# Performance work log

Hardware: AMD Instinct MI355X
Metric: run time of the kernel (lower is better)

Reference implementation:

```python
import jax, jax.numpy as jnp
import numpy as np

_BN = 1.0 / np.sqrt(1.0 + 1e-5)  # eval-mode BatchNorm1d with default (fresh-init) stats/affine

def bn(z):
    return z * _BN

def lrelu(z, a):
    return jnp.where(z >= 0, z, a * z)

NEG = -9e15

def setup_inputs() -> dict:
    key = jax.random.key(0)
    ks = jax.random.split(key, 20)
    H = Wd = 256; B = 200; N = 2048; NHID = 128; OUT = 64; HEADS = 4
    x = jax.random.normal(ks[0], (H, Wd, B), dtype=jnp.float32)
    Q = jax.random.uniform(ks[1], (H * Wd, N), dtype=jnp.float32)
    adj = (jax.random.uniform(ks[2], (N, N)) < 0.02).astype(jnp.float32)
    adj = jnp.maximum(adj, jnp.eye(N, dtype=jnp.float32))  # self loops so no empty rows
    def u(k, shape, fan):
        s = 1.0 / np.sqrt(fan)
        return jax.random.uniform(k, shape, jnp.float32, -s, s)
    inp = dict(x=x, adj=adj, Q=Q)
    inp['g1a_W'] = u(ks[3], (B, NHID), NHID);  inp['g1a_b'] = u(ks[4], (NHID,), NHID)
    inp['g1b_W'] = u(ks[5], (NHID, B), B);     inp['g1b_b'] = u(ks[6], (B,), B)
    inp['g2a_W'] = u(ks[7], (B, NHID), NHID);  inp['g2a_b'] = u(ks[8], (NHID,), NHID)
    inp['g2b_W'] = u(ks[9], (NHID, OUT), OUT); inp['g2b_b'] = u(ks[10], (OUT,), OUT)
    inp['gat_W'] = jax.random.normal(ks[11], (HEADS, B, NHID)) * 0.1
    inp['gat_a'] = jax.random.normal(ks[12], (HEADS, 2 * NHID)) * 0.1
    inp['out_W'] = jax.random.normal(ks[13], (HEADS * NHID, OUT)) * 0.1
    inp['out_a'] = jax.random.normal(ks[14], (2 * OUT,)) * 0.1
    inp['Wf'] = u(ks[15], (2, OUT), OUT)
    inp['bf'] = u(ks[16], (2, OUT), OUT)
    inp['conv_w'] = jax.random.normal(ks[17], (3,)) * 0.5
    inp['conv_b'] = jax.random.normal(ks[18], (1,)) * 0.1
    return inp

def reference(x, adj, Q, g1a_W, g1a_b, g1b_W, g1b_b, g2a_W, g2a_b, g2b_W, g2b_b,
              gat_W, gat_a, out_W, out_a, Wf, bf, conv_w, conv_b):
    HW = x.shape[0] * x.shape[1]
    xf = x.reshape(HW, -1)                                   # [HW, C]
    normQ = Q / jnp.sum(Q, axis=0, keepdims=True)            # column-normalized assignment
    sp = normQ.T @ xf                                        # [N, C] superpixel features
    xn = bn(sp)

    # ---- Res_GCN branch ----
    def gcn_block(z, Wa, ba, Wb, bb):
        z = bn(z)
        z = lrelu(adj @ (z @ Wa) + ba, 0.01)
        z = bn(z)
        return adj @ (z @ Wb) + bb

    xg = bn(xn)
    y = lrelu(bn(gcn_block(xg, g1a_W, g1a_b, g1b_W, g1b_b)), 0.01)
    xg = xg + y
    GCN_x = lrelu(bn(gcn_block(xg, g2a_W, g2a_b, g2b_W, g2b_b)), 0.01)  # [N, OUT]

    # ---- GAT branch (fused pairwise scores: e_ij = lrelu(a1.Wh_i + a2.Wh_j)) ----
    mask = adj > 0
    nhid = gat_W.shape[2]

    def gat_head(Wk, ak):
        Wh = xn @ Wk                                         # [N, nhid]
        f1 = Wh @ ak[:nhid]                                  # [N]
        f2 = Wh @ ak[nhid:]                                  # [N]
        e = lrelu(f1[:, None] + f2[None, :], 0.2)            # [N, N]
        att = jax.nn.softmax(jnp.where(mask, e, NEG), axis=1)
        return jax.nn.elu(att @ Wh)                          # concat=True -> ELU

    heads = jax.vmap(gat_head)(gat_W, gat_a)                 # [H, N, nhid]
    hcat = jnp.moveaxis(heads, 0, 1).reshape(heads.shape[1], -1)  # [N, H*nhid]

    fo = out_W.shape[1]
    Wh = hcat @ out_W                                        # [N, OUT]
    e = lrelu((Wh @ out_a[:fo])[:, None] + (Wh @ out_a[fo:])[None, :], 0.2)
    att = jax.nn.softmax(jnp.where(mask, e, NEG), axis=1)
    GAT_x = lrelu(bn(jax.nn.elu(att @ Wh)), 0.01)            # [N, OUT]

    # ---- adaptive fusion ----
    mn = jnp.minimum(GCN_x, GAT_x)
    mx = jnp.maximum(GCN_x, GAT_x)
    avg = (GCN_x * Wf[0] + bf[0]) + (GAT_x * Wf[1] + bf[1])
    stk = jnp.stack([mn, mx, avg], axis=0)                   # [3, N, OUT]
    inp3 = stk + GAT_x + GCN_x                               # broadcast add
    y = jnp.einsum('c,cnf->nf', conv_w, inp3) + conv_b       # 1x1 conv 3->1 channels
    y = lrelu(bn(y), 0.2)                                    # AF2GNN1 leakyrelu(alpha)
    return Q @ y                                             # [HW, OUT]
```

## Files before the change

kernel.cpp:

```cpp
#include <hip/hip_runtime.h>
#include <math.h>

#define BNF 0.9999950000374997f

constexpr int N    = 2048;
constexpr int C    = 200;
constexpr int HW   = 65536;
constexpr int MAXDEG = 96;

typedef unsigned short u16;
typedef __attribute__((ext_vector_type(8))) short short8;
typedef __attribute__((ext_vector_type(4))) float f32x4;

union Frag  { short8 v; ushort4 h[2]; };
union FragA { short8 v; uint2 u2[2]; };

__device__ inline u16 f2bf(float x) {
    unsigned int u = __float_as_uint(x);
    unsigned int r = (u + 0x7fffu + ((u >> 16) & 1u)) >> 16;
    return (u16)r;
}

__device__ __forceinline__ void gload16(const void* g, void* l) {
    __builtin_amdgcn_global_load_lds(
        (const __attribute__((address_space(1))) unsigned int*)g,
        (__attribute__((address_space(3))) unsigned int*)l, 16, 0, 0);
}

__global__ __launch_bounds__(256) void k_convX(const float* __restrict__ xf,
                                               u16* __restrict__ xfT) {
    __shared__ __align__(16) u16 T2[200][140];
    const int i0 = blockIdx.x * 128;
    const int t = threadIdx.x;
    for (int p = 0; p < 25; ++p) {
        int idx = p * 256 + t;
        int il = idx / 50, cq = idx % 50;
        float4 v = *(const float4*)&xf[(size_t)(i0 + il) * 200 + cq * 4];
        T2[cq * 4 + 0][il] = f2bf(v.x);
        T2[cq * 4 + 1][il] = f2bf(v.y);
        T2[cq * 4 + 2][il] = f2bf(v.z);
        T2[cq * 4 + 3][il] = f2bf(v.w);
    }
    __syncthreads();
    for (int p = 0; p < 13; ++p) {
        int c = p * 16 + (t >> 4);
        if (c < 200) {
            int io = (t & 15) * 8;
            u16* dst = &xfT[(size_t)c * 65536 + i0 + io];
            *(ushort4*)&dst[0] = *(const ushort4*)&T2[c][io];
            *(ushort4*)&dst[4] = *(const ushort4*)&T2[c][io + 4];
        }
    }
    ushort4 z4 = {0, 0, 0, 0};
    for (int idx = t; idx < 8 * 16; idx += 256) {
        int r = 200 + (idx >> 4), io = (idx & 15) * 8;
        u16* dst = &xfT[(size_t)r * 65536 + i0 + io];
        *(ushort4*)&dst[0] = z4;
        *(ushort4*)&dst[4] = z4;
    }
}

__global__ __launch_bounds__(256, 3) void k_bigS(const float* __restrict__ Q,
                                                 const u16* __restrict__ xfT,
                                                 u16* __restrict__ Qbf,
                                                 float* __restrict__ S_part,
                                                 float* __restrict__ csPart) {
    __shared__ __align__(16) u16 Bt[2][208 * 32];
    __shared__ __align__(16) u16 At[64 * 34];
    const int bid = blockIdx.x;
    const int xcd = bid & 7, jb = bid >> 3;
    const int nt_b = jb & 31;
    const int ks_b = ((jb >> 5) << 3) + xcd;
    const int n0 = nt_b * 64;
    const size_t i0 = (size_t)ks_b * 2048;
    const int t = threadIdx.x, w = t >> 6, l = t & 63;
    const int ct0 = (w == 0) ? 0 : (4 + (w - 1) * 3);
    const int nct = (w == 0) ? 4 : 3;
    const int lrowB = l >> 2;
    const int scolB = (((l & 3) ^ ((l >> 3) & 3)) << 3);
    const int nq = t & 15;
    const int kp = t >> 4;

    f32x4 acc[4][4];
#pragma unroll
    for (int a = 0; a < 4; ++a)
#pragma unroll
        for (int b = 0; b < 4; ++b) acc[a][b] = (f32x4){0.f, 0.f, 0.f, 0.f};
    float csum[4] = {0.f, 0.f, 0.f, 0.f};

    float4 aq0, ar0, aq1, ar1;

#define ISSUE_B(PAR, STEP)                                                      \
    {                                                                           \
        const size_t kc = i0 + (size_t)(STEP) * 32 + scolB;                     \
        for (int s = w; s < 13; s += 4)                                         \
            gload16(&xfT[(size_t)(s * 16 + lrowB) * 65536 + kc],                \
                    &Bt[PAR][s * 512]);                                         \
    }

#define LOAD_A(AQ, AR, STEP)                                                    \
    {                                                                           \
        const float* qp = &Q[(i0 + (size_t)(STEP) * 32 + kp * 2) * 2048         \
                             + n0 + nq * 4];                                    \
        AQ = *(const float4*)qp;                                                \
        AR = *(const float4*)(qp + 2048);                                       \
    }

#define WRITE_A(AQ, AR, STEP)                                                   \
    {                                                                           \
        const float* ca = (const float*)&AQ;                                    \
        const float* cb = (const float*)&AR;                                    \
        ushort4 s0, s1;                                                         \
        u16* q0 = (u16*)&s0; u16* q1 = (u16*)&s1;                               \
        _Pragma("unroll")                                                       \
        for (int jj = 0; jj < 4; ++jj) {                                        \
            const int n_ = nq * 4 + jj;                                         \
            ushort2 p2;                                                         \
            p2.x = f2bf(ca[jj]); p2.y = f2bf(cb[jj]);                           \
            *(ushort2*)&At[n_ * 34 + ((n_ & 1) << 1) + kp * 2] = p2;            \
            csum[jj] += ca[jj] + cb[jj];                                        \
            q0[jj] = p2.x; q1[jj] = p2.y;                                       \
        }                                                                       \
        const size_t r0 = i0 + (size_t)(STEP) * 32 + kp * 2;                    \
        *(ushort4*)&Qbf[r0 * 2048 + n0 + nq * 4] = s0;                          \
        *(ushort4*)&Qbf[(r0 + 1) * 2048 + n0 + nq * 4] = s1;                    \
    }

#define MFMA_PHASE(PAR)                                                         \
    {                                                                           \
        const u16* Bb = Bt[PAR];                                                \
        const int g = l >> 4;                                                   \
        FragA af[4];                                                            \
        _Pragma("unroll")                                                       \
        for (int nt = 0; nt < 4; ++nt) {                                        \
            const int r = nt * 16 + (l & 15);                                   \
            const int ab = r * 34 + ((r & 1) << 1) + g * 8;                     \
            af[nt].u2[0] = *(const uint2*)&At[ab];                              \
            af[nt].u2[1] = *(const uint2*)&At[ab + 4];                          \
        }                                                                       \
        _Pragma("unroll")                                                       \
        for (int c = 0; c < 4; ++c) {                                           \
            if (c < nct) {                                                      \
                const int rb = (ct0 + c) * 16 + (l & 15);                       \
                Frag bf;                                                        \
                bf.v = *(const short8*)&Bb[rb * 32 + ((g ^ ((rb >> 1) & 3)) << 3)]; \
                _Pragma("unroll")                                               \
                for (int nt = 0; nt < 4; ++nt)                                  \
                    acc[nt][c] = __builtin_amdgcn_mfma_f32_16x16x32_bf16(       \
                        af[nt].v, bf.v, acc[nt][c], 0, 0, 0);                   \
            }                                                                   \
        }                                                                       \
    }

#define STEPBODY(STEP, PAR, NPAR, CQ, CR, NQr, NRr, COND)                       \
    {                                                                           \
        if (COND) ISSUE_B(NPAR, (STEP) + 1);                                    \
        WRITE_A(CQ, CR, STEP);                                                  \
        if (COND) LOAD_A(NQr, NRr, (STEP) + 1);                                 \
        asm volatile("s_waitcnt lgkmcnt(0)" ::: "memory");                      \
        __builtin_amdgcn_s_barrier();                                           \
        if (COND) {                                                             \
            if (w == 0) asm volatile("s_waitcnt vmcnt(8)" ::: "memory");        \
            else        asm volatile("s_waitcnt vmcnt(7)" ::: "memory");        \
        } else {                                                                \
            asm volatile("s_waitcnt vmcnt(0)" ::: "memory");                    \
        }                                                                       \
        MFMA_PHASE(PAR);                                                        \
        __builtin_amdgcn_s_barrier();                                           \
    }

    ISSUE_B(0, 0);
    LOAD_A(aq0, ar0, 0);

    for (int s2 = 0; s2 < 32; ++s2) {
        STEPBODY(s2 * 2,     0, 1, aq0, ar0, aq1, ar1, true);
        STEPBODY(s2 * 2 + 1, 1, 0, aq1, ar1, aq0, ar0, (s2 < 31));
    }
#undef STEPBODY
#undef MFMA_PHASE
#undef WRITE_A
#undef LOAD_A
#undef ISSUE_B

    __syncthreads();
    float* csF = (float*)At;
#pragma unroll
    for (int jj = 0; jj < 4; ++jj)
        csF[kp * 64 + nq * 4 + jj] = csum[jj];
    __syncthreads();
    if (t < 64) {
        float s = 0.f;
#pragma unroll
        for (int g2 = 0; g2 < 16; ++g2) s += csF[g2 * 64 + t];
        csPart[(size_t)ks_b * 2048 + n0 + t] = s;
    }
    float* Sp = S_part + (size_t)ks_b * 409600;
#pragma unroll
    for (int nt = 0; nt < 4; ++nt)
#pragma unroll
        for (int c = 0; c < 4; ++c) {
            if (c < nct) {
                const int cc = (ct0 + c) * 16 + (l & 15);
                if (cc < 200) {
                    const int nbase = n0 + nt * 16 + ((l >> 4) << 2);
#pragma unroll
                    for (int r = 0; r < 4; ++r)
                        Sp[(size_t)(nbase + r) * 200 + cc] = acc[nt][c][r];
                }
            }
        }
}

__global__ void k_redS(const float* __restrict__ S_part, const float* __restrict__ csPart,
                       float* __restrict__ xn, float* __restrict__ xg) {
    int i = blockIdx.x * 256 + threadIdx.x;
    if (i >= N * C) return;
    int n = i / C;
    float s = 0.f, csn = 0.f;
#pragma unroll 8
    for (int p = 0; p < 32; ++p) s += S_part[(size_t)p * 409600 + i];
#pragma unroll 8
    for (int p = 0; p < 32; ++p) csn += csPart[(size_t)p * 2048 + n];
    float v = BNF * s / csn;
    xn[i] = v;
    xg[i] = BNF * v;
}

__global__ void k_csr(const float* __restrict__ adj, int* __restrict__ deg,
                      int* __restrict__ idxs) {
    int w = threadIdx.x >> 6, lane = threadIdx.x & 63;
    int n = blockIdx.x * 4 + w;
    const float* row = adj + (size_t)n * N;
    int base = 0;
    for (int c = 0; c < N; c += 64) {
        float v = row[c + lane];
        bool p = v > 0.f;
        unsigned long long m = __ballot(p);
        int pos = __popcll(m & ((1ull << lane) - 1ull));
        if (p && (base + pos) < MAXDEG) idxs[(size_t)n * MAXDEG + base + pos] = c + lane;
        base += __popcll(m);
    }
    if (lane == 0) deg[n] = base < MAXDEG ? base : MAXDEG;
}

__global__ __launch_bounds__(256) void k_mm(const float* __restrict__ A,
                                            const float* __restrict__ W,
                                            float* __restrict__ Cc,
                                            int K, int Wout, int ostride,
                                            int zc_off, int zw_str, float scale) {
    __shared__ float ldsA[32][33];
    __shared__ float ldsW[32][64];
    const int rt = blockIdx.x * 32;
    const int ct = blockIdx.y * 64;
    const int z  = blockIdx.z;
    const float* Wp = W + (size_t)z * zw_str;
    const int coff = z * zc_off;
    const int t = threadIdx.x;
    const int lane = t & 63, wg = t >> 6;
    float acc[8];
#pragma unroll
    for (int r = 0; r < 8; ++r) acc[r] = 0.f;

    for (int k0 = 0; k0 < K; k0 += 32) {
        for (int idx = t; idx < 32 * 32; idx += 256) {
            int r = idx >> 5, kk = idx & 31;
            int k = k0 + kk;
            ldsA[r][kk] = (k < K) ? A[(size_t)(rt + r) * K + k] : 0.f;
        }
        for (int idx = t; idx < 32 * 64; idx += 256) {
            int kk = idx >> 6, c = idx & 63;
            int k = k0 + kk, cg = ct + c;
            ldsW[kk][c] = (k < K && cg < Wout) ? Wp[(size_t)k * Wout + cg] : 0.f;
        }
        __syncthreads();
#pragma unroll 8
        for (int kk = 0; kk < 32; ++kk) {
            float wv = ldsW[kk][lane];
#pragma unroll
            for (int r = 0; r < 8; ++r) acc[r] += ldsA[wg * 8 + r][kk] * wv;
        }
        __syncthreads();
    }
    int cg = ct + lane;
    if (cg < Wout) {
#pragma unroll
        for (int r = 0; r < 8; ++r)
            Cc[(size_t)(rt + wg * 8 + r) * ostride + coff + cg] = scale * acc[r];
    }
}

__global__ void k_spmm(const float* __restrict__ h, const int* __restrict__ deg,
                       const int* __restrict__ idxs, const float* __restrict__ bias,
                       const float* __restrict__ res, float* __restrict__ out,
                       int W, float s, int act) {
    int n = blockIdx.x;
    int d = deg[n];
    const int* row = idxs + (size_t)n * MAXDEG;
    int k0 = threadIdx.x;
    int k1 = threadIdx.x + 128;
    float a0 = 0.f, a1 = 0.f;
    for (int j = 0; j < d; ++j) {
        const float* hr = h + (size_t)row[j] * W;
        a0 += hr[k0];
        if (k1 < W) a1 += hr[k1];
    }
    {
        float v = s * (a0 + bias[k0]);
        if (act) v = v >= 0.f ? v : 0.01f * v;
        if (res) v += res[(size_t)n * W + k0];
        out[(size_t)n * W + k0] = v;
    }
    if (k1 < W) {
        float v = s * (a1 + bias[k1]);
        if (act) v = v >= 0.f ? v : 0.01f * v;
        if (res) v += res[(size_t)n * W + k1];
        out[(size_t)n * W + k1] = v;
    }
}

__global__ __launch_bounds__(256) void k_wh5(const float* __restrict__ xn,
                                             const float* __restrict__ gatW,
                                             const float* __restrict__ gata,
                                             const float* __restrict__ g1aW,
                                             float* __restrict__ WhB,
                                             float* __restrict__ f1,
                                             float* __restrict__ f2,
                                             float* __restrict__ hbuf) {
    __shared__ float ldsA[32][33];
    __shared__ float ldsW[32][128];
    __shared__ float ldsWh[32][129];
    const int rt = blockIdx.x * 32;
    const int z  = blockIdx.y;
    const bool gat = z < 4;
    const float* Wp = gat ? gatW + (size_t)z * 25600 : g1aW;
    const int t = threadIdx.x;
    const int col = t & 127, rg = t >> 7;
    float acc[16];
#pragma unroll
    for (int r = 0; r < 16; ++r) acc[r] = 0.f;

    for (int k0 = 0; k0 < 200; k0 += 32) {
        for (int idx = t; idx < 32 * 32; idx += 256) {
            int r = idx >> 5, kk = idx & 31;
            int k = k0 + kk;
            ldsA[r][kk] = (k < 200) ? xn[(size_t)(rt + r) * 200 + k] : 0.f;
        }
        for (int idx = t; idx < 32 * 128; idx += 256) {
            int kk = idx >> 7, c = idx & 127;
            int k = k0 + kk;
            ldsW[kk][c] = (k < 200) ? Wp[(size_t)k * 128 + c] : 0.f;
        }
        __syncthreads();
#pragma unroll 8
        for (int kk = 0; kk < 32; ++kk) {
            float wv = ldsW[kk][col];
#pragma unroll
            for (int r = 0; r < 16; ++r) acc[r] += ldsA[rg * 16 + r][kk] * wv;
        }
        __syncthreads();
    }
    if (gat) {
#pragma unroll
        for (int r = 0; r < 16; ++r) {
            ldsWh[rg * 16 + r][col] = acc[r];
            WhB[(size_t)(rt + rg * 16 + r) * 512 + z * 128 + col] = acc[r];
        }
        __syncthreads();
        int row = t >> 3, p = t & 7;
        const float* a = gata + z * 256;
        float s1 = 0.f, s2 = 0.f;
#pragma unroll
        for (int j = 0; j < 16; ++j) {
            int c = p * 16 + j;
            float v = ldsWh[row][c];
            s1 += v * a[c]; s2 += v * a[128 + c];
        }
        s1 += __shfl_xor(s1, 1); s1 += __shfl_xor(s1, 2); s1 += __shfl_xor(s1, 4);
        s2 += __shfl_xor(s2, 1); s2 += __shfl_xor(s2, 2); s2 += __shfl_xor(s2, 4);
        if (p == 0) { f1[z * N + rt + row] = s1; f2[z * N + rt + row] = s2; }
    } else {
        const float sc = BNF * BNF;
#pragma unroll
        for (int r = 0; r < 16; ++r)
            hbuf[(size_t)(rt + rg * 16 + r) * 128 + col] = sc * acc[r];
    }
}

__global__ void k_att_head(const float* __restrict__ WhB, const float* __restrict__ f1,
                           const float* __restrict__ f2, const int* __restrict__ deg,
                           const int* __restrict__ idxs, float* __restrict__ hcat) {
    __shared__ float eW[MAXDEG];
    int n = blockIdx.x, h = blockIdx.y;
    int k = threadIdx.x;
    int d = deg[n];
    const int* row = idxs + (size_t)n * MAXDEG;
    float f1v = f1[h * N + n];
    const float* f2h = f2 + h * N;
    if (k < d) {
        float e = f1v + f2h[row[k]];
        eW[k] = e >= 0.f ? e : 0.2f * e;
    }
    __syncthreads();
    float mx = -1e30f;
    for (int j = 0; j < d; ++j) mx = fmaxf(mx, eW[j]);
    __syncthreads();
    if (k < d) eW[k] = __expf(eW[k] - mx);
    __syncthreads();
    float ssum = 0.f, acc = 0.f;
    for (int j = 0; j < d; ++j) ssum += eW[j];
    for (int j = 0; j < d; ++j)
        acc += eW[j] * WhB[(size_t)row[j] * 512 + h * 128 + k];
    float v = acc / ssum;
    v = v > 0.f ? v : __expf(v) - 1.f;
    hcat[(size_t)n * 512 + h * 128 + k] = v;
}

__global__ __launch_bounds__(256) void k_mmO(const float* __restrict__ hcat,
                                             const float* __restrict__ outW,
                                             const float* __restrict__ outa,
                                             float* __restrict__ WhO,
                                             float* __restrict__ f1o,
                                             float* __restrict__ f2o) {
    __shared__ float ldsA[32][33];
    __shared__ float ldsW[32][64];
    const int rt = blockIdx.x * 32;
    const int t = threadIdx.x;
    const int lane = t & 63, wg = t >> 6;
    float acc[8];
#pragma unroll
    for (int r = 0; r < 8; ++r) acc[r] = 0.f;

    for (int k0 = 0; k0 < 512; k0 += 32) {
        for (int idx = t; idx < 32 * 32; idx += 256) {
            int r = idx >> 5, kk = idx & 31;
            ldsA[r][kk] = hcat[(size_t)(rt + r) * 512 + k0 + kk];
        }
        for (int idx = t; idx < 32 * 64; idx += 256) {
            int kk = idx >> 6, c = idx & 63;
            ldsW[kk][c] = outW[(size_t)(k0 + kk) * 64 + c];
        }
        __syncthreads();
#pragma unroll 8
        for (int kk = 0; kk < 32; ++kk) {
            float wv = ldsW[kk][lane];
#pragma unroll
            for (int r = 0; r < 8; ++r) acc[r] += ldsA[wg * 8 + r][kk] * wv;
        }
        __syncthreads();
    }
#pragma unroll
    for (int r = 0; r < 8; ++r)
        WhO[(size_t)(rt + wg * 8 + r) * 64 + lane] = acc[r];
#pragma unroll
    for (int r = 0; r < 8; ++r) {
        float v1 = acc[r] * outa[lane];
        float v2 = acc[r] * outa[64 + lane];
#pragma unroll
        for (int off = 32; off; off >>= 1) {
            v1 += __shfl_down(v1, off);
            v2 += __shfl_down(v2, off);
        }
        if (lane == 0) { f1o[rt + wg * 8 + r] = v1; f2o[rt + wg * 8 + r] = v2; }
    }
}

__global__ void k_att_out(const float* __restrict__ WhO, const float* __restrict__ f1o,
                          const float* __restrict__ f2o, const int* __restrict__ deg,
                          const int* __restrict__ idxs, const float* __restrict__ GCNx,
                          const float* __restrict__ Wf, const float* __restrict__ bfp,
                          const float* __restrict__ cw, const float* __restrict__ cb,
                          u16* __restrict__ yT) {
    __shared__ float eW[MAXDEG];
    int n = blockIdx.x;
    int k = threadIdx.x;
    int d = deg[n];
    const int* row = idxs + (size_t)n * MAXDEG;
    float f1v = f1o[n];
    for (int j = k; j < d; j += 64) {
        float e = f1v + f2o[row[j]];
        eW[j] = e >= 0.f ? e : 0.2f * e;
    }
    __syncthreads();
    float mx = -1e30f;
    for (int j = 0; j < d; ++j) mx = fmaxf(mx, eW[j]);
    __syncthreads();
    for (int j = k; j < d; j += 64) eW[j] = __expf(eW[j] - mx);
    __syncthreads();
    float ssum = 0.f, acc = 0.f;
    for (int j = 0; j < d; ++j) ssum += eW[j];
    for (int j = 0; j < d; ++j)
        acc += eW[j] * WhO[(size_t)row[j] * 64 + k];
    float v = acc / ssum;
    v = v > 0.f ? v : __expf(v) - 1.f;
    v *= BNF;
    float gat = v >= 0.f ? v : 0.01f * v;
    float g = GCNx[(size_t)n * 64 + k];
    float mn = fminf(g, gat), mxv = fmaxf(g, gat);
    float avg = g * Wf[k] + bfp[k] + gat * Wf[64 + k] + bfp[64 + k];
    float base = g + gat;
    float yv = cw[0] * (mn + base) + cw[1] * (mxv + base) + cw[2] * (avg + base) + cb[0];
    yv *= BNF;
    yv = yv >= 0.f ? yv : 0.2f * yv;
    yT[k * 2048 + n] = f2bf(yv);
}

__global__ __launch_bounds__(256, 3) void k_final(const u16* __restrict__ Qbf,
                                                  const u16* __restrict__ yT,
                                                  float* __restrict__ out) {
    __shared__ __align__(16) u16 Aq[2][128 * 64];
    __shared__ __align__(16) u16 By[2][64 * 64];
    const int i0 = blockIdx.x * 128;
    const int t = threadIdx.x, w = t >> 6, l = t & 63;
    const int lrow = l >> 3;
    const int scol = (((l & 7) ^ ((l >> 3) & 7)) << 3);
    f32x4 acc[2][4];
#pragma unroll
    for (int a = 0; a < 2; ++a)
#pragma unroll
        for (int b = 0; b < 4; ++b) acc[a][b] = (f32x4){0.f, 0.f, 0.f, 0.f};

#define STAGE_F(buf, step)                                                          \
    {                                                                               \
        const size_t kc = (size_t)(step) * 64 + scol;                               \
        for (int s = w; s < 16; s += 4)                                             \
            gload16(&Qbf[(size_t)(i0 + s * 8 + lrow) * 2048 + kc],                  \
                    &Aq[buf][s * 512]);                                             \
        for (int s = w; s < 8; s += 4)                                              \
            gload16(&yT[(size_t)(s * 8 + lrow) * 2048 + kc],                        \
                    &By[buf][s * 512]);                                             \
    }

    STAGE_F(0, 0);
    for (int step = 0; step < 32; ++step) {
        const int cur = step & 1;
        if (step + 1 < 32) {
            STAGE_F(cur ^ 1, step + 1);
            asm volatile("s_waitcnt vmcnt(6)" ::: "memory");
        } else {
            asm volatile("s_waitcnt vmcnt(0)" ::: "memory");
        }
        __builtin_amdgcn_s_barrier();

        const u16* Ab = Aq[cur];
        const u16* Bb = By[cur];
#pragma unroll
        for (int sub = 0; sub < 2; ++sub) {
            const int c8 = sub * 4 + (l >> 4);
            Frag a[2];
#pragma unroll
            for (int it = 0; it < 2; ++it) {
                const int r = w * 32 + it * 16 + (l & 15);
                a[it].v = *(const short8*)&Ab[r * 64 + ((c8 ^ (r & 7)) << 3)];
            }
#pragma unroll
            for (int ft = 0; ft < 4; ++ft) {
                const int rb = ft * 16 + (l & 15);
                Frag b;
                b.v = *(const short8*)&Bb[rb * 64 + ((c8 ^ (rb & 7)) << 3)];
#pragma unroll
                for (int it = 0; it < 2; ++it)
                    acc[it][ft] = __builtin_amdgcn_mfma_f32_16x16x32_bf16(
                        a[it].v, b.v, acc[it][ft], 0, 0, 0);
            }
        }
        asm volatile("s_waitcnt lgkmcnt(0)" ::: "memory");
        __builtin_amdgcn_s_barrier();
    }
#undef STAGE_F
#pragma unroll
    for (int it = 0; it < 2; ++it)
#pragma unroll
        for (int ft = 0; ft < 4; ++ft) {
            const int i = i0 + w * 32 + it * 16 + ((l >> 4) << 2);
            const int f = ft * 16 + (l & 15);
#pragma unroll
            for (int r = 0; r < 4; ++r)
                out[(size_t)(i + r) * 64 + f] = acc[it][ft][r];
        }
}

extern "C" void kernel_launch(void* const* d_in, const int* in_sizes, int n_in,
                              void* d_out, int out_size, void* d_ws, size_t ws_size,
                              hipStream_t stream) {
    const float* x     = (const float*)d_in[0];
    const float* adj   = (const float*)d_in[1];
    const float* Q     = (const float*)d_in[2];
    const float* g1aW  = (const float*)d_in[3];
    const float* g1ab  = (const float*)d_in[4];
    const float* g1bW  = (const float*)d_in[5];
    const float* g1bb  = (const float*)d_in[6];
    const float* g2aW  = (const float*)d_in[7];
    const float* g2ab  = (const float*)d_in[8];
    const float* g2bW  = (const float*)d_in[9];
    const float* g2bb  = (const float*)d_in[10];
    const float* gatW  = (const float*)d_in[11];
    const float* gata  = (const float*)d_in[12];
    const float* outW  = (const float*)d_in[13];
    const float* outa  = (const float*)d_in[14];
    const float* Wf    = (const float*)d_in[15];
    const float* bfp   = (const float*)d_in[16];
    const float* convw = (const float*)d_in[17];
    const float* convb = (const float*)d_in[18];

    float* ws   = (float*)d_ws;
    float* xn   = ws + 411648;
    float* xg   = ws + 821248;
    float* xg2  = ws + 1230848;
    float* hbuf = ws + 1640448;
    float* zbuf = ws + 2050048;
    float* WhO  = ws + 2312192;
    float* GCNx = ws + 2443264;
    float* f1   = ws + 2836480;
    float* f2   = ws + 2844672;
    float* f1o  = ws + 2852864;
    float* f2o  = ws + 2854912;
    int*   deg  = (int*)(ws + 2856960);
    int*   idxs = (int*)(ws + 2859008);
    u16*   yT   = (u16*)(ws + 1640448);
    float* csPart = ws + 3000000;
    float* S_part = ws + 4200000;
    u16*   Qbf    = (u16*)(ws + 71308864);
    u16*   xfT    = (u16*)(ws + 138417728);

    float* out  = (float*)d_out;
    float* WhB  = out;
    float* hcat = out + 1048576;

    k_convX<<<512, 256, 0, stream>>>(x, xfT);
    k_bigS<<<1024, 256, 0, stream>>>(Q, xfT, Qbf, S_part, csPart);
    k_redS<<<(N * C + 255) / 256, 256, 0, stream>>>(S_part, csPart, xn, xg);
    k_csr<<<N / 4, 256, 0, stream>>>(adj, deg, idxs);

    k_wh5<<<dim3(64, 5), 256, 0, stream>>>(xn, gatW, gata, g1aW, WhB, f1, f2, hbuf);

    k_spmm<<<N, 128, 0, stream>>>(hbuf, deg, idxs, g1ab, nullptr, zbuf, 128, 1.f, 1);
    k_att_head<<<dim3(N, 4), 128, 0, stream>>>(WhB, f1, f2, deg, idxs, hcat);
    k_mm<<<dim3(64, 4, 1), 256, 0, stream>>>(zbuf, g1bW, hbuf, 128, 200, 200, 0, 0, BNF);
    k_mmO<<<64, 256, 0, stream>>>(hcat, outW, outa, WhO, f1o, f2o);
    k_spmm<<<N, 128, 0, stream>>>(hbuf, deg, idxs, g1bb, xg, xg2, 200, BNF, 1);
    k_mm<<<dim3(64, 2, 1), 256, 0, stream>>>(xg2, g2aW, hbuf, 200, 128, 128, 0, 0, BNF);
    k_spmm<<<N, 128, 0, stream>>>(hbuf, deg, idxs, g2ab, nullptr, zbuf, 128, 1.f, 1);
    k_mm<<<dim3(64, 1, 1), 256, 0, stream>>>(zbuf, g2bW, hbuf, 128, 64, 64, 0, 0, BNF);
    k_spmm<<<N, 64, 0, stream>>>(hbuf, deg, idxs, g2bb, nullptr, GCNx, 64, BNF, 1);

    k_att_out<<<N, 64, 0, stream>>>(WhO, f1o, f2o, deg, idxs, GCNx,
                                    Wf, bfp, convw, convb, yT);

    k_final<<<512, 256, 0, stream>>>(Qbf, yT, out);
}
```

Before: 724.6 us.

## Deepen load prefetch in bigS and final GEMMs, fuse redS and csr kernels

In k_bigS, the A-operand register prefetch now runs two steps ahead instead of one, with wider vmcnt waits, so global loads have more time to land before they are consumed. In k_final, the LDS staging goes from double to triple buffering with matching waitcnt levels, and occupancy is lowered from 3 to 2 blocks per SM to make room for the larger shared buffers. k_redS and k_csr are merged into a single launch that dispatches on block index, which removes one kernel launch and lets the two independent jobs overlap. The risks are higher register and LDS pressure, lower occupancy in k_final, and subtle errors in the waitcnt accounting or in the reuse of the aq/ar register buffers.

```diff
diff --git a/kernel.cpp b/kernel.cpp
--- a/kernel.cpp
+++ b/kernel.cpp
@@ -152,16 +152,19 @@
         }                                                                       \
     }
 
-#define STEPBODY(STEP, PAR, NPAR, CQ, CR, NQr, NRr, COND)                       \
+#define STEPBODY(STEP, PAR, NPAR, CQ, CR, COND)                                 \
     {                                                                           \
         if (COND) ISSUE_B(NPAR, (STEP) + 1);                                    \
         WRITE_A(CQ, CR, STEP);                                                  \
-        if (COND) LOAD_A(NQr, NRr, (STEP) + 1);                                 \
+        {                                                                       \
+            const int nst = ((STEP) + 2 > 63) ? 63 : (STEP) + 2;                \
+            LOAD_A(CQ, CR, nst);                                                \
+        }                                                                       \
         asm volatile("s_waitcnt lgkmcnt(0)" ::: "memory");                      \
         __builtin_amdgcn_s_barrier();                                           \
         if (COND) {                                                             \
-            if (w == 0) asm volatile("s_waitcnt vmcnt(8)" ::: "memory");        \
-            else        asm volatile("s_waitcnt vmcnt(7)" ::: "memory");        \
+            if (w == 0) asm volatile("s_waitcnt vmcnt(12)" ::: "memory");       \
+            else        asm volatile("s_waitcnt vmcnt(11)" ::: "memory");       \
         } else {                                                                \
             asm volatile("s_waitcnt vmcnt(0)" ::: "memory");                    \
         }                                                                       \
@@ -171,10 +174,11 @@
 
     ISSUE_B(0, 0);
     LOAD_A(aq0, ar0, 0);
+    LOAD_A(aq1, ar1, 1);
 
     for (int s2 = 0; s2 < 32; ++s2) {
-        STEPBODY(s2 * 2,     0, 1, aq0, ar0, aq1, ar1, true);
-        STEPBODY(s2 * 2 + 1, 1, 0, aq1, ar1, aq0, ar0, (s2 < 31));
+        STEPBODY(s2 * 2,     0, 1, aq0, ar0, true);
+        STEPBODY(s2 * 2 + 1, 1, 0, aq1, ar1, (s2 < 31));
     }
 #undef STEPBODY
 #undef MFMA_PHASE
@@ -211,36 +215,38 @@
         }
 }
 
-__global__ void k_redS(const float* __restrict__ S_part, const float* __restrict__ csPart,
-                       float* __restrict__ xn, float* __restrict__ xg) {
-    int i = blockIdx.x * 256 + threadIdx.x;
-    if (i >= N * C) return;
-    int n = i / C;
-    float s = 0.f, csn = 0.f;
+__global__ void k_aux(const float* __restrict__ S_part, const float* __restrict__ csPart,
+                      float* __restrict__ xn, float* __restrict__ xg,
+                      const float* __restrict__ adj, int* __restrict__ deg,
+                      int* __restrict__ idxs) {
+    const int bid = blockIdx.x;
+    if (bid < 1600) {
+        int i = bid * 256 + threadIdx.x;
+        if (i >= N * C) return;
+        int n = i / C;
+        float s = 0.f, csn = 0.f;
 #pragma unroll 8
-    for (int p = 0; p < 32; ++p) s += S_part[(size_t)p * 409600 + i];
+        for (int p = 0; p < 32; ++p) s += S_part[(size_t)p * 409600 + i];
 #pragma unroll 8
-    for (int p = 0; p < 32; ++p) csn += csPart[(size_t)p * 2048 + n];
-    float v = BNF * s / csn;
-    xn[i] = v;
-    xg[i] = BNF * v;
-}
-
-__global__ void k_csr(const float* __restrict__ adj, int* __restrict__ deg,
-                      int* __restrict__ idxs) {
-    int w = threadIdx.x >> 6, lane = threadIdx.x & 63;
-    int n = blockIdx.x * 4 + w;
-    const float* row = adj + (size_t)n * N;
-    int base = 0;
-    for (int c = 0; c < N; c += 64) {
-        float v = row[c + lane];
-        bool p = v > 0.f;
-        unsigned long long m = __ballot(p);
-        int pos = __popcll(m & ((1ull << lane) - 1ull));
-        if (p && (base + pos) < MAXDEG) idxs[(size_t)n * MAXDEG + base + pos] = c + lane;
-        base += __popcll(m);
-    }
-    if (lane == 0) deg[n] = base < MAXDEG ? base : MAXDEG;
+        for (int p = 0; p < 32; ++p) csn += csPart[(size_t)p * 2048 + n];
+        float v = BNF * s / csn;
+        xn[i] = v;
+        xg[i] = BNF * v;
+    } else {
+        int w = threadIdx.x >> 6, lane = threadIdx.x & 63;
+        int n = (bid - 1600) * 4 + w;
+        const float* row = adj + (size_t)n * N;
+        int base = 0;
+        for (int c = 0; c < N; c += 64) {
+            float v = row[c + lane];
+            bool p = v > 0.f;
+            unsigned long long m = __ballot(p);
+            int pos = __popcll(m & ((1ull << lane) - 1ull));
+            if (p && (base + pos) < MAXDEG) idxs[(size_t)n * MAXDEG + base + pos] = c + lane;
+            base += __popcll(m);
+        }
+        if (lane == 0) deg[n] = base < MAXDEG ? base : MAXDEG;
+    }
 }
 
 __global__ __launch_bounds__(256) void k_mm(const float* __restrict__ A,
@@ -504,11 +510,11 @@
     yT[k * 2048 + n] = f2bf(yv);
 }
 
-__global__ __launch_bounds__(256, 3) void k_final(const u16* __restrict__ Qbf,
+__global__ __launch_bounds__(256, 2) void k_final(const u16* __restrict__ Qbf,
                                                   const u16* __restrict__ yT,
                                                   float* __restrict__ out) {
-    __shared__ __align__(16) u16 Aq[2][128 * 64];
-    __shared__ __align__(16) u16 By[2][64 * 64];
+    __shared__ __align__(16) u16 Aq[3][128 * 64];
+    __shared__ __align__(16) u16 By[3][64 * 64];
     const int i0 = blockIdx.x * 128;
     const int t = threadIdx.x, w = t >> 6, l = t & 63;
     const int lrow = l >> 3;
@@ -531,14 +537,13 @@
     }
 
     STAGE_F(0, 0);
+    STAGE_F(1, 1);
     for (int step = 0; step < 32; ++step) {
-        const int cur = step & 1;
-        if (step + 1 < 32) {
-            STAGE_F(cur ^ 1, step + 1);
-            asm volatile("s_waitcnt vmcnt(6)" ::: "memory");
-        } else {
-            asm volatile("s_waitcnt vmcnt(0)" ::: "memory");
-        }
+        const int cur = step % 3;
+        if (step + 2 < 32) STAGE_F((step + 2) % 3, step + 2);
+        if (step + 2 < 32)      asm volatile("s_waitcnt vmcnt(12)" ::: "memory");
+        else if (step + 1 < 32) asm volatile("s_waitcnt vmcnt(6)"  ::: "memory");
+        else                    asm volatile("s_waitcnt vmcnt(0)"  ::: "memory");
         __builtin_amdgcn_s_barrier();
 
         const u16* Ab = Aq[cur];
@@ -628,8 +633,7 @@
 
     k_convX<<<512, 256, 0, stream>>>(x, xfT);
     k_bigS<<<1024, 256, 0, stream>>>(Q, xfT, Qbf, S_part, csPart);
-    k_redS<<<(N * C + 255) / 256, 256, 0, stream>>>(S_part, csPart, xn, xg);
-    k_csr<<<N / 4, 256, 0, stream>>>(adj, deg, idxs);
+    k_aux<<<2112, 256, 0, stream>>>(S_part, csPart, xn, xg, adj, deg, idxs);
 
     k_wh5<<<dim3(64, 5), 256, 0, stream>>>(xn, gatW, gata, g1aW, WhB, f1, f2, hbuf);
 
```

Result: faster. 694.5 us (-4.2%).
